# Optimization experiments

Hardware: AMD Instinct MI355X
Metric: run time of the kernel (lower is better)

The kernel has to match this reference:

```python
import jax, jax.numpy as jnp
import numpy as np

B, IN, H, OUT = 128, 256, 128, 32

def setup_inputs() -> dict:
    key = jax.random.key(0)
    ks = jax.random.split(key, 7)
    return {
        "input": jax.random.normal(ks[0], (B, IN), dtype=jnp.float32),
        "sigma_psi": jax.random.normal(ks[1], (1, IN, H, OUT), dtype=jnp.float32),
        "chi": jax.random.normal(ks[2], (1, IN, H, 1), dtype=jnp.float32),
        "sigma_eps": jax.random.normal(ks[3], (1, H, OUT), dtype=jnp.float32),
        "eta": jax.random.normal(ks[4], (1, H, OUT), dtype=jnp.float32),
        "mu_phi": jax.random.normal(ks[5], (1, OUT), dtype=jnp.float32),
        "sigma_phi": jax.random.normal(ks[6], (1, OUT), dtype=jnp.float32),
    }

def reference(input, sigma_psi, chi, sigma_eps, eta, mu_phi, sigma_phi):
    # x: (B, IN, 1, 1); broadcast diff against chi (1, IN, H, 1)
    x = input.reshape(-1, input.shape[1], 1, 1)
    # s: (B, H, OUT) = sum over in_features of (sigma_psi*(chi-x))^2
    s = jnp.sum((sigma_psi * (chi - x)) ** 2, axis=1)
    w = 1.0 / (s + sigma_eps ** 2)                       # (B, H, OUT)
    denom = 1.0 + sigma_phi ** 2 * jnp.sum(w, axis=1)    # (B, OUT)
    post_mu = (mu_phi + sigma_phi ** 2 * jnp.sum(w * eta, axis=1)) / denom
    post_sigma2 = sigma_phi ** 2 / denom
    return post_mu, post_sigma2
```

## Files before the change

### kernel.cpp

```cpp
#include <hip/hip_runtime.h>

#define B_   128
#define IN_  256
#define H_   128
#define OUT_ 32
#define HT   4
#define BT   8
#define NHB  (H_ / HT)
#define NBB  (B_ / BT)
#define DIFF_STRIDE 2056
#define SM_FLOATS   (HT * DIFF_STRIDE)

__global__ __launch_bounds__(256, 2) void o1u_main(
    const float* __restrict__ input,
    const float* __restrict__ sigma_psi,
    const float* __restrict__ chi,
    const float* __restrict__ sigma_eps,
    const float* __restrict__ eta,
    float* __restrict__ sw_part,
    float* __restrict__ swe_part)
{
    const int tid = threadIdx.x;
    const int ig = tid >> 5;
    const int hl = (tid >> 3) & 3;
    const int og = tid & 7;
    const int hb = blockIdx.x;
    const int h_base = hb * HT;
    const int b_base = blockIdx.y * BT;

    __shared__ __align__(16) float sm[SM_FLOATS];

#pragma unroll
    for (int k = 0; k < (HT * IN_ * BT) / 256; ++k) {
        int flat = k * 256 + tid;
        int b  = flat & 7;
        int i  = (flat >> 3) & 255;
        int hh = flat >> 11;
        float e = chi[i * H_ + (h_base + hh)] - input[(b_base + b) * IN_ + i];
        sm[hh * DIFF_STRIDE + (flat & 2047)] = e * e;
    }
    __syncthreads();

    const float* sp_base = sigma_psi + (size_t)(h_base + hl) * OUT_ + og * 4;
    const float* drow = sm + hl * DIFF_STRIDE;
    float s[BT][4];
#pragma unroll
    for (int b = 0; b < BT; ++b)
#pragma unroll
        for (int j = 0; j < 4; ++j) s[b][j] = 0.0f;

#pragma unroll 4
    for (int k = 0; k < IN_ / 8; ++k) {
        int i = ig * 32 + k;
        float4 sp = *(const float4*)(sp_base + (size_t)i * (H_ * OUT_));
        float4 sp2;
        sp2.x = sp.x * sp.x; sp2.y = sp.y * sp.y;
        sp2.z = sp.z * sp.z; sp2.w = sp.w * sp.w;
        const float4* dp = (const float4*)(drow + i * 8);
        float4 eA = dp[0];
        float4 eB = dp[1];
        float ev[8] = {eA.x, eA.y, eA.z, eA.w, eB.x, eB.y, eB.z, eB.w};
#pragma unroll
        for (int b = 0; b < BT; ++b) {
            s[b][0] = fmaf(sp2.x, ev[b], s[b][0]);
            s[b][1] = fmaf(sp2.y, ev[b], s[b][1]);
            s[b][2] = fmaf(sp2.z, ev[b], s[b][2]);
            s[b][3] = fmaf(sp2.w, ev[b], s[b][3]);
        }
    }

    __syncthreads();
#pragma unroll
    for (int b = 0; b < BT; ++b) {
        float4 v; v.x = s[b][0]; v.y = s[b][1]; v.z = s[b][2]; v.w = s[b][3];
        *(float4*)(sm + ig * 1024 + hl * 256 + b * 32 + og * 4) = v;
    }
    __syncthreads();

    const int rb = tid >> 5;
    const int ro = tid & 31;
    float sw = 0.0f, swe = 0.0f;
#pragma unroll
    for (int hh = 0; hh < HT; ++hh) {
        float sfull = 0.0f;
#pragma unroll
        for (int g = 0; g < 8; ++g)
            sfull += sm[g * 1024 + hh * 256 + rb * 32 + ro];
        float se = sigma_eps[(h_base + hh) * OUT_ + ro];
        float w = 1.0f / fmaf(se, se, sfull);
        sw += w;
        swe += w * eta[(h_base + hh) * OUT_ + ro];
    }
    sw_part[((size_t)hb * B_ + (b_base + rb)) * OUT_ + ro] = sw;
    swe_part[((size_t)hb * B_ + (b_base + rb)) * OUT_ + ro] = swe;
}

__global__ __launch_bounds__(64) void o1u_final(
    const float* __restrict__ sw_part,
    const float* __restrict__ swe_part,
    const float* __restrict__ mu_phi,
    const float* __restrict__ sigma_phi,
    float* __restrict__ out)
{
    const int idx = blockIdx.x * 64 + threadIdx.x;
    const int o = idx & (OUT_ - 1);
    float sw = 0.0f, swe = 0.0f;
#pragma unroll 8
    for (int hb = 0; hb < NHB; ++hb) {
        sw  += sw_part[hb * (B_ * OUT_) + idx];
        swe += swe_part[hb * (B_ * OUT_) + idx];
    }
    float sp = sigma_phi[o];
    float sp2 = sp * sp;
    float inv = 1.0f / fmaf(sp2, sw, 1.0f);
    out[idx] = fmaf(sp2, swe, mu_phi[o]) * inv;
    out[B_ * OUT_ + idx] = sp2 * inv;
}

extern "C" void kernel_launch(void* const* d_in, const int* in_sizes, int n_in,
                              void* d_out, int out_size, void* d_ws, size_t ws_size,
                              hipStream_t stream) {
    const float* input     = (const float*)d_in[0];
    const float* sigma_psi = (const float*)d_in[1];
    const float* chi       = (const float*)d_in[2];
    const float* sigma_eps = (const float*)d_in[3];
    const float* eta       = (const float*)d_in[4];
    const float* mu_phi    = (const float*)d_in[5];
    const float* sigma_phi = (const float*)d_in[6];
    float* out = (float*)d_out;
    float* ws  = (float*)d_ws;

    float* sw_part  = ws;
    float* swe_part = ws + NHB * B_ * OUT_;

    dim3 grid(NHB, NBB);
    o1u_main<<<grid, 256, 0, stream>>>(input, sigma_psi, chi, sigma_eps, eta,
                                       sw_part, swe_part);
    o1u_final<<<(B_ * OUT_) / 64, 64, 0, stream>>>(sw_part, swe_part,
                                                   mu_phi, sigma_phi, out);
}
```

Before: 79.12 us.

## Halve H tile, split IN across 16 groups, parallelize final reduction

The H tile shrinks from 4 to 2, doubling the grid to 64x16 blocks, and the IN reduction is split across 16 thread groups of 16 inputs each instead of 8 groups of 32. Shared memory is padded per group to avoid bank conflicts. The diff prologue is restructured so each thread loads its chi pair and 8 inputs once. The final kernel now uses 4 lanes per output combined by shuffles, since there are twice as many partials. More partial sums and more blocks raise parallelism and occupancy at the cost of extra workspace traffic and less reuse of each diff tile.

Result: faster. 75.36 us (-4.8%).

```diff
diff --git a/kernel.cpp b/kernel.cpp
--- a/kernel.cpp
+++ b/kernel.cpp
@@ -4,14 +4,14 @@
 #define IN_  256
 #define H_   128
 #define OUT_ 32
-#define HT   4
+#define HT   2
 #define BT   8
 #define NHB  (H_ / HT)
 #define NBB  (B_ / BT)
-#define DIFF_STRIDE 2056
-#define SM_FLOATS   (HT * DIFF_STRIDE)
+#define DIFF_STRIDE 2184
+#define SM_FLOATS   8192
 
-__global__ __launch_bounds__(256, 2) void o1u_main(
+__global__ __launch_bounds__(256, 4) void o2_main(
     const float* __restrict__ input,
     const float* __restrict__ sigma_psi,
     const float* __restrict__ chi,
@@ -21,42 +21,58 @@
     float* __restrict__ swe_part)
 {
     const int tid = threadIdx.x;
-    const int ig = tid >> 5;
-    const int hl = (tid >> 3) & 3;
     const int og = tid & 7;
+    const int hl = (tid >> 3) & 1;
+    const int ig = tid >> 4;
     const int hb = blockIdx.x;
     const int h_base = hb * HT;
     const int b_base = blockIdx.y * BT;
 
     __shared__ __align__(16) float sm[SM_FLOATS];
 
+    {
+        const int i = tid;
+        const float2 c2 = *(const float2*)(chi + i * H_ + h_base);
+        float xv[8];
 #pragma unroll
-    for (int k = 0; k < (HT * IN_ * BT) / 256; ++k) {
-        int flat = k * 256 + tid;
-        int b  = flat & 7;
-        int i  = (flat >> 3) & 255;
-        int hh = flat >> 11;
-        float e = chi[i * H_ + (h_base + hh)] - input[(b_base + b) * IN_ + i];
-        sm[hh * DIFF_STRIDE + (flat & 2047)] = e * e;
+        for (int b = 0; b < 8; ++b)
+            xv[b] = input[(b_base + b) * IN_ + i];
+        const int ioff = i * 8 + (i >> 4) * 8;
+#pragma unroll
+        for (int hh = 0; hh < HT; ++hh) {
+            const float c = (hh == 0) ? c2.x : c2.y;
+            float4 w0, w1; float e;
+            e = c - xv[0]; w0.x = e * e;
+            e = c - xv[1]; w0.y = e * e;
+            e = c - xv[2]; w0.z = e * e;
+            e = c - xv[3]; w0.w = e * e;
+            e = c - xv[4]; w1.x = e * e;
+            e = c - xv[5]; w1.y = e * e;
+            e = c - xv[6]; w1.z = e * e;
+            e = c - xv[7]; w1.w = e * e;
+            float* dst = sm + hh * DIFF_STRIDE + ioff;
+            *(float4*)dst       = w0;
+            *(float4*)(dst + 4) = w1;
+        }
     }
     __syncthreads();
 
-    const float* sp_base = sigma_psi + (size_t)(h_base + hl) * OUT_ + og * 4;
-    const float* drow = sm + hl * DIFF_STRIDE;
+    const float* sp_ptr = sigma_psi + (size_t)(h_base + hl) * OUT_ + og * 4;
+    const float* drow = sm + hl * DIFF_STRIDE + ig * 136;
     float s[BT][4];
 #pragma unroll
-    for (int b = 0; b < BT; ++b)
-#pragma unroll
-        for (int j = 0; j < 4; ++j) s[b][j] = 0.0f;
+    for (int b = 0; b < BT; ++b) {
+        s[b][0] = 0.f; s[b][1] = 0.f; s[b][2] = 0.f; s[b][3] = 0.f;
+    }
 
 #pragma unroll 4
-    for (int k = 0; k < IN_ / 8; ++k) {
-        int i = ig * 32 + k;
-        float4 sp = *(const float4*)(sp_base + (size_t)i * (H_ * OUT_));
+    for (int k = 0; k < 16; ++k) {
+        const int i = ig * 16 + k;
+        float4 sp = *(const float4*)(sp_ptr + (size_t)i * (H_ * OUT_));
         float4 sp2;
         sp2.x = sp.x * sp.x; sp2.y = sp.y * sp.y;
         sp2.z = sp.z * sp.z; sp2.w = sp.w * sp.w;
-        const float4* dp = (const float4*)(drow + i * 8);
+        const float4* dp = (const float4*)(drow + k * 8);
         float4 eA = dp[0];
         float4 eB = dp[1];
         float ev[8] = {eA.x, eA.y, eA.z, eA.w, eB.x, eB.y, eB.z, eB.w};
@@ -73,7 +89,7 @@
 #pragma unroll
     for (int b = 0; b < BT; ++b) {
         float4 v; v.x = s[b][0]; v.y = s[b][1]; v.z = s[b][2]; v.w = s[b][3];
-        *(float4*)(sm + ig * 1024 + hl * 256 + b * 32 + og * 4) = v;
+        *(float4*)(sm + ig * 512 + hl * 256 + b * 32 + og * 4) = v;
     }
     __syncthreads();
 
@@ -84,37 +100,45 @@
     for (int hh = 0; hh < HT; ++hh) {
         float sfull = 0.0f;
 #pragma unroll
-        for (int g = 0; g < 8; ++g)
-            sfull += sm[g * 1024 + hh * 256 + rb * 32 + ro];
-        float se = sigma_eps[(h_base + hh) * OUT_ + ro];
-        float w = 1.0f / fmaf(se, se, sfull);
+        for (int g = 0; g < 16; ++g)
+            sfull += sm[g * 512 + hh * 256 + rb * 32 + ro];
+        const float se = sigma_eps[(h_base + hh) * OUT_ + ro];
+        const float w = 1.0f / fmaf(se, se, sfull);
         sw += w;
         swe += w * eta[(h_base + hh) * OUT_ + ro];
     }
-    sw_part[((size_t)hb * B_ + (b_base + rb)) * OUT_ + ro] = sw;
-    swe_part[((size_t)hb * B_ + (b_base + rb)) * OUT_ + ro] = swe;
+    const size_t po = ((size_t)hb * B_ + (b_base + rb)) * OUT_ + ro;
+    sw_part[po]  = sw;
+    swe_part[po] = swe;
 }
 
-__global__ __launch_bounds__(64) void o1u_final(
+__global__ __launch_bounds__(256) void o2_final(
     const float* __restrict__ sw_part,
     const float* __restrict__ swe_part,
     const float* __restrict__ mu_phi,
     const float* __restrict__ sigma_phi,
     float* __restrict__ out)
 {
-    const int idx = blockIdx.x * 64 + threadIdx.x;
-    const int o = idx & (OUT_ - 1);
+    const int g = blockIdx.x * 256 + threadIdx.x;
+    const int bin = g >> 2;
+    const int q = g & 3;
     float sw = 0.0f, swe = 0.0f;
-#pragma unroll 8
-    for (int hb = 0; hb < NHB; ++hb) {
-        sw  += sw_part[hb * (B_ * OUT_) + idx];
-        swe += swe_part[hb * (B_ * OUT_) + idx];
+#pragma unroll
+    for (int k = 0; k < NHB / 4; ++k) {
+        const int hb = q * (NHB / 4) + k;
+        sw  += sw_part[hb * (B_ * OUT_) + bin];
+        swe += swe_part[hb * (B_ * OUT_) + bin];
     }
-    float sp = sigma_phi[o];
-    float sp2 = sp * sp;
-    float inv = 1.0f / fmaf(sp2, sw, 1.0f);
-    out[idx] = fmaf(sp2, swe, mu_phi[o]) * inv;
-    out[B_ * OUT_ + idx] = sp2 * inv;
+    sw  += __shfl_xor(sw, 1);   swe += __shfl_xor(swe, 1);
+    sw  += __shfl_xor(sw, 2);   swe += __shfl_xor(swe, 2);
+    if (q == 0) {
+        const int o = bin & (OUT_ - 1);
+        const float sp = sigma_phi[o];
+        const float sp2 = sp * sp;
+        const float inv = 1.0f / fmaf(sp2, sw, 1.0f);
+        out[bin] = fmaf(sp2, swe, mu_phi[o]) * inv;
+        out[B_ * OUT_ + bin] = sp2 * inv;
+    }
 }
 
 extern "C" void kernel_launch(void* const* d_in, const int* in_sizes, int n_in,
@@ -134,8 +158,8 @@
     float* swe_part = ws + NHB * B_ * OUT_;
 
     dim3 grid(NHB, NBB);
-    o1u_main<<<grid, 256, 0, stream>>>(input, sigma_psi, chi, sigma_eps, eta,
-                                       sw_part, swe_part);
-    o1u_final<<<(B_ * OUT_) / 64, 64, 0, stream>>>(sw_part, swe_part,
-                                                   mu_phi, sigma_phi, out);
+    o2_main<<<grid, 256, 0, stream>>>(input, sigma_psi, chi, sigma_eps, eta,
+                                      sw_part, swe_part);
+    o2_final<<<(B_ * OUT_ * 4) / 256, 256, 0, stream>>>(sw_part, swe_part,
+                                                        mu_phi, sigma_phi, out);
 }
```
